# Optimization experiments

Hardware: AMD Instinct MI355X
Metric: run time of the kernel (lower is better)

Reference implementation:

```python
import jax, jax.numpy as jnp
import numpy as np

N = 20000    # num nodes
E = 320000   # num edges (also rows of edge_type, SPN line-graph style)
F = 64       # num_features
HID = 64     # hidden_channels
HEADS = 4    # gatv2_heads
NC = 2       # num_classes
PH = 128     # proxy hidden size
SLOPE = 0.2  # PyG GATv2 leaky_relu negative slope


def gatv2(feat, src, dst, wl, wr, att, b, num_nodes, concat):
    # GATv2Conv (PyG semantics, add_self_loops=True, dropout off in eval)
    H, C = att.shape
    xl = (feat @ wl).reshape(-1, H, C)
    xr = (feat @ wr).reshape(-1, H, C)
    loops = jnp.arange(num_nodes, dtype=src.dtype)
    s = jnp.concatenate([src, loops])
    d = jnp.concatenate([dst, loops])
    e = jax.nn.leaky_relu(xl[s] + xr[d], SLOPE)            # [E', H, C]
    logits = jnp.einsum('ehc,hc->eh', e, att)              # [E', H]
    m = jax.ops.segment_max(logits, d, num_segments=num_nodes)
    p = jnp.exp(logits - m[d])
    z = jax.ops.segment_sum(p, d, num_segments=num_nodes)
    alpha = p / z[d]                                       # segment softmax
    out = jax.ops.segment_sum(xl[s] * alpha[:, :, None], d, num_segments=num_nodes)
    out = out.reshape(num_nodes, H * C) if concat else out.mean(axis=1)
    return out + b


def setup_inputs():
    key = jax.random.key(0)
    ks = iter(jax.random.split(key, 32))
    def rn(shape, scale=0.1):
        return jax.random.normal(next(ks), shape, dtype=jnp.float32) * scale
    return {
        'x': rn((N, F), 1.0),
        'edge_type': rn((E, F), 1.0),
        'edge_index': jax.random.randint(next(ks), (2, E), 0, N, dtype=jnp.int32),
        'n1_wl': rn((F, HEADS * HID)), 'n1_wr': rn((F, HEADS * HID)),
        'n1_att': rn((HEADS, HID)), 'n1_b': jnp.zeros((HEADS * HID,), jnp.float32),
        'n2_wl': rn((HEADS * HID, HID)), 'n2_wr': rn((HEADS * HID, HID)),
        'n2_att': rn((1, HID)), 'n2_b': jnp.zeros((HID,), jnp.float32),
        'e1_wl': rn((F, HEADS * HID)), 'e1_wr': rn((F, HEADS * HID)),
        'e1_att': rn((HEADS, HID)), 'e1_b': jnp.zeros((HEADS * HID,), jnp.float32),
        'e2_wl': rn((HEADS * HID, HID)), 'e2_wr': rn((HEADS * HID, HID)),
        'e2_att': rn((1, HID)), 'e2_b': jnp.zeros((HID,), jnp.float32),
        'crf_wu': rn((HID, NC)), 'crf_bu': jnp.zeros((NC,), jnp.float32),
        'crf_wp': rn((HID, NC)),
        'px_w1': rn((HID, PH)), 'px_b1': jnp.zeros((PH,), jnp.float32),
        'px_w2': rn((PH, NC)), 'px_b2': jnp.zeros((NC,), jnp.float32),
    }


def reference(x, edge_type, edge_index, n1_wl, n1_wr, n1_att, n1_b, n2_wl, n2_wr, n2_att, n2_b,
              e1_wl, e1_wr, e1_att, e1_b, e2_wl, e2_wr, e2_att, e2_b,
              crf_wu, crf_bu, crf_wp, px_w1, px_b1, px_w2, px_b2):
    src, dst = edge_index[0], edge_index[1]
    # node GNN: GATv2 -> ELU -> GATv2 (dropout = identity in eval)
    h = jax.nn.elu(gatv2(x, src, dst, n1_wl, n1_wr, n1_att, n1_b, N, True))
    node_repr = gatv2(h, src, dst, n2_wl, n2_wr, n2_att, n2_b, N, False)
    # edge GNN over edge features (E rows, same edge_index, per source code)
    g = jax.nn.elu(gatv2(edge_type, src, dst, e1_wl, e1_wr, e1_att, e1_b, E, True))
    edge_repr = gatv2(g, src, dst, e2_wl, e2_wr, e2_att, e2_b, E, False)
    # CRF head: unary potentials + pairwise messages scattered to dst nodes
    unary = node_repr @ crf_wu + crf_bu
    msg = jax.ops.segment_sum(edge_repr @ crf_wp, dst, num_segments=N)
    crf_out = jax.nn.log_softmax(unary + msg, axis=-1)
    # MLP proxy head
    ph = jax.nn.relu(node_repr @ px_w1 + px_b1)
    proxy_out = ph @ px_w2 + px_b2
    return crf_out, proxy_out
```

## Files before the change

kernel.cpp:

```cpp
#include <hip/hip_runtime.h>
#include <cstddef>
#include <cstdint>

#define N_NODES 20000
#define N_EDGES 320000

typedef __attribute__((ext_vector_type(8))) short bf8_t;
typedef __attribute__((ext_vector_type(4))) float f4_t;
typedef __attribute__((ext_vector_type(2))) float f2_t;
typedef unsigned short bfu;
typedef _Float16 half_t;
typedef __attribute__((ext_vector_type(2))) _Float16 h2_t;
typedef __attribute__((ext_vector_type(4))) _Float16 h4_t;
typedef __attribute__((ext_vector_type(8))) _Float16 h8_t;

__device__ __forceinline__ short f2bf(float f) {
  unsigned u = __float_as_uint(f);
  u += 0x7fff + ((u >> 16) & 1);
  return (short)(u >> 16);
}
__device__ __forceinline__ h2_t leaky_h2(h2_t t) {
  h2_t zero = {(_Float16)0.f, (_Float16)0.f};
  h2_t mx = __builtin_elementwise_max(t, zero);
  h2_t mn = __builtin_elementwise_min(t, zero);
  h2_t c  = {(_Float16)0.2f, (_Float16)0.2f};
  return mn * c + mx;
}
__device__ __forceinline__ float dot2h(h2_t a, h2_t b, float c) {
#if __has_builtin(__builtin_amdgcn_fdot2)
  return __builtin_amdgcn_fdot2(a, b, c, false);
#else
  return c + (float)a.x * (float)b.x + (float)a.y * (float)b.y;
#endif
}

__global__ void count_deg_kernel(const int* __restrict__ dst, int* __restrict__ deg, int e_cnt) {
  int e = blockIdx.x * blockDim.x + threadIdx.x;
  if (e < e_cnt) atomicAdd(&deg[dst[e]], 1);
}

__global__ __launch_bounds__(1024) void scan_kernel(
    const int* __restrict__ deg, int* __restrict__ rowptr,
    int* __restrict__ cursor, int n) {
  __shared__ int sdata[1024];
  const int CH = (n + 1023) / 1024;
  int tid = threadIdx.x;
  int base = tid * CH;
  int loc[20];
  int s = 0;
  for (int j = 0; j < CH; ++j) {
    int idx = base + j;
    int v = (idx < n) ? deg[idx] : 0;
    loc[j] = s;
    s += v;
  }
  sdata[tid] = s;
  __syncthreads();
  for (int off = 1; off < 1024; off <<= 1) {
    int t = (tid >= off) ? sdata[tid - off] : 0;
    __syncthreads();
    sdata[tid] += t;
    __syncthreads();
  }
  int excl = sdata[tid] - s;
  for (int j = 0; j < CH; ++j) {
    int idx = base + j;
    if (idx < n) { int val = excl + loc[j]; rowptr[idx] = val; cursor[idx] = val; }
  }
  if (tid == 0) rowptr[n] = sdata[1023];
}

__global__ void fill_csr_kernel(const int* __restrict__ src, const int* __restrict__ dst,
                                int* __restrict__ cursor, int* __restrict__ csr_src,
                                int* __restrict__ csr_eid, int e_cnt) {
  int e = blockIdx.x * blockDim.x + threadIdx.x;
  if (e < e_cnt) {
    int pos = atomicAdd(&cursor[dst[e]], 1);
    csr_src[pos] = src[e];
    csr_eid[pos] = e;
  }
}

__global__ void prep_all_kernel(
    const float* __restrict__ n1l, const float* __restrict__ n1r,
    const float* __restrict__ e1l, const float* __restrict__ e1r,
    const float* __restrict__ n2l, const float* __restrict__ n2r,
    const float* __restrict__ e2l, const float* __restrict__ e2r,
    const float* __restrict__ b2, const float* __restrict__ wp,
    short* __restrict__ t_n1l, short* __restrict__ t_n1r,
    short* __restrict__ t_e1l, short* __restrict__ t_e1r,
    short* __restrict__ t_n2l, short* __restrict__ t_n2r,
    short* __restrict__ t_e2l, short* __restrict__ t_e2r,
    float* __restrict__ wct, float* __restrict__ pc)
{
  int i = blockIdx.x * blockDim.x + threadIdx.x;
  int seg = i >> 14;
  int j = i & 16383;
  if (seg < 4) {
    const float* srcs[4] = {n1l, n1r, e1l, e1r};
    short* dsts[4] = {t_n1l, t_n1r, t_e1l, t_e1r};
    int n = j >> 6, k = j & 63;
    dsts[seg][n * 64 + k] = f2bf(srcs[seg][k * 256 + n]);
  } else if (seg < 8) {
    const float* srcs[4] = {n2l, n2r, e2l, e2r};
    short* dsts[4] = {t_n2l, t_n2r, t_e2l, t_e2r};
    int n = j >> 8, k = j & 255;
    dsts[seg - 4][n * 256 + k] = f2bf(srcs[seg - 4][k * 64 + n]);
  } else if (seg == 8) {
    if (j < 512) {
      int jj = j & 1;
      int k  = j >> 1;
      float s = 0.f;
      for (int c = 0; c < 64; ++c) s = fmaf(e2l[k * 64 + c], wp[c * 2 + jj], s);
      wct[jj * 256 + k] = s;
    } else if (j < 514) {
      int jj = j - 512;
      float s = 0.f;
      for (int c = 0; c < 64; ++c) s = fmaf(b2[c], wp[c * 2 + jj], s);
      pc[jj] = s;
    }
  }
}

template<int K>
__global__ __launch_bounds__(128) void mfma_proj2_kernel(
    const float* __restrict__ A0,
    const short* __restrict__ Wtl0, const short* __restrict__ Wtr0,
    half_t* __restrict__ xl0, half_t* __restrict__ xr0,
    const float* __restrict__ A1,
    const short* __restrict__ Wtl1, const short* __restrict__ Wtr1,
    half_t* __restrict__ xl1, half_t* __restrict__ xr1,
    int M, int nslices)
{
  constexpr int KC = K / 32;
  int tid = threadIdx.x;
  int w = tid >> 6, lane = tid & 63, quad = lane >> 4, l15 = lane & 15;
  int row_base = (int)blockIdx.x * 64 + w * 32;
  int y = (int)blockIdx.y;
  int z = (int)blockIdx.z;
  const float* A = z ? A1 : A0;
  bool is_l = y < nslices;
  const short* Wt = z ? (is_l ? Wtl1 : Wtr1) : (is_l ? Wtl0 : Wtr0);
  half_t* dst = z ? (is_l ? xl1 : xr1) : (is_l ? xl0 : xr0);
  int cb = (is_l ? y : y - nslices) * 64;
  int STR = nslices * 64;

  bf8_t a[2][KC];
  #pragma unroll
  for (int rt = 0; rt < 2; ++rt) {
    int r = row_base + rt * 16 + l15;
    int rc = r < M ? r : M - 1;
    const float* ap = A + (size_t)rc * K + quad * 8;
    #pragma unroll
    for (int kc = 0; kc < KC; ++kc) {
      float4 v0 = *(const float4*)(ap + kc * 32);
      float4 v1 = *(const float4*)(ap + kc * 32 + 4);
      bf8_t f;
      f[0] = f2bf(v0.x); f[1] = f2bf(v0.y); f[2] = f2bf(v0.z); f[3] = f2bf(v0.w);
      f[4] = f2bf(v1.x); f[5] = f2bf(v1.y); f[6] = f2bf(v1.z); f[7] = f2bf(v1.w);
      a[rt][kc] = f;
    }
  }

  #pragma unroll
  for (int nt = 0; nt < 4; ++nt) {
    f4_t acc0 = {0.f, 0.f, 0.f, 0.f};
    f4_t acc1 = {0.f, 0.f, 0.f, 0.f};
    const short* wb = Wt + (size_t)(cb + nt * 16 + l15) * K + quad * 8;
    #pragma unroll
    for (int kc = 0; kc < KC; ++kc) {
      bf8_t wf = *(const bf8_t*)(wb + kc * 32);
      acc0 = __builtin_amdgcn_mfma_f32_16x16x32_bf16(wf, a[0][kc], acc0, 0, 0, 0);
      acc1 = __builtin_amdgcn_mfma_f32_16x16x32_bf16(wf, a[1][kc], acc1, 0, 0, 0);
    }
    #pragma unroll
    for (int rt = 0; rt < 2; ++rt) {
      f4_t acc = rt == 0 ? acc0 : acc1;
      int row = row_base + rt * 16 + l15;
      if (row >= M) continue;
      int col = cb + nt * 16 + quad * 4;
      h4_t pk;
      pk[0] = (_Float16)acc[0]; pk[1] = (_Float16)acc[1];
      pk[2] = (_Float16)acc[2]; pk[3] = (_Float16)acc[3];
      *(h4_t*)&dst[(size_t)row * STR + col] = pk;
    }
  }
}

template<int KIN>
__device__ __forceinline__ void gemm_body(
    const float* __restrict__ A, const float* __restrict__ W, int wld, int cb,
    int block_m, int M, float (&acc)[8][4],
    float (*As)[128 + 4], float (*Ws)[64 + 4])
{
  int tid = threadIdx.x;
  int tx = tid & 15;
  int ty = tid >> 4;
  #pragma unroll
  for (int i = 0; i < 8; ++i)
    #pragma unroll
    for (int j = 0; j < 4; ++j) acc[i][j] = 0.f;

  for (int k0 = 0; k0 < KIN; k0 += 16) {
    #pragma unroll
    for (int rep = 0; rep < 2; ++rep) {
      int ar = (tid >> 2) + rep * 64;
      int ak = (tid & 3) * 4;
      int gr = block_m + ar;
      float4 v = make_float4(0.f, 0.f, 0.f, 0.f);
      if (gr < M) v = *(const float4*)&A[(size_t)gr * KIN + k0 + ak];
      As[ak + 0][ar] = v.x; As[ak + 1][ar] = v.y;
      As[ak + 2][ar] = v.z; As[ak + 3][ar] = v.w;
    }
    {
      int wr = tid >> 4;
      int wc = (tid & 15) * 4;
      float4 v = *(const float4*)&W[(size_t)(k0 + wr) * wld + cb + wc];
      Ws[wr][wc + 0] = v.x; Ws[wr][wc + 1] = v.y;
      Ws[wr][wc + 2] = v.z; Ws[wr][wc + 3] = v.w;
    }
    __syncthreads();
    #pragma unroll
    for (int k = 0; k < 16; ++k) {
      float a[8], w[4];
      #pragma unroll
      for (int i = 0; i < 8; ++i) a[i] = As[k][ty * 8 + i];
      #pragma unroll
      for (int j = 0; j < 4; ++j) w[j] = Ws[k][tx * 4 + j];
      #pragma unroll
      for (int i = 0; i < 8; ++i)
        #pragma unroll
        for (int j = 0; j < 4; ++j) acc[i][j] = fmaf(a[i], w[j], acc[i][j]);
    }
    __syncthreads();
  }
}

template<int KIN, int MODE>
__global__ __launch_bounds__(256) void gemm64_kernel(
    const float* __restrict__ A, const float* __restrict__ W, int wld,
    const float* __restrict__ bias, float* __restrict__ out, int old, int M)
{
  __shared__ float As[16][128 + 4];
  __shared__ float Ws[16][64 + 4];
  float acc[8][4];
  int block_m = (int)blockIdx.x * 128;
  int cb = (int)blockIdx.y * 64;
  gemm_body<KIN>(A, W, wld, cb, block_m, M, acc, As, Ws);

  int tid = threadIdx.x;
  int tx = tid & 15, ty = tid >> 4;
  int gc = cb + tx * 4;
  #pragma unroll
  for (int i = 0; i < 8; ++i) {
    int gr = block_m + ty * 8 + i;
    if (gr >= M) continue;
    size_t idx = (size_t)gr * old + gc;
    float t0 = acc[i][0], t1 = acc[i][1], t2 = acc[i][2], t3 = acc[i][3];
    if (MODE == 3) {
      t0 = fmaxf(t0 + bias[gc + 0], 0.f);
      t1 = fmaxf(t1 + bias[gc + 1], 0.f);
      t2 = fmaxf(t2 + bias[gc + 2], 0.f);
      t3 = fmaxf(t3 + bias[gc + 3], 0.f);
    }
    *(float4*)&out[idx] = make_float4(t0, t1, t2, t3);
  }
}

template<int STR, bool ELU, bool FUSEP>
__global__ __launch_bounds__(256) void gat_agg_v6(
    const half_t* __restrict__ xl0, const half_t* __restrict__ xr0,
    const float* __restrict__ att0, const float* __restrict__ bias0,
    float* __restrict__ out0,
    const half_t* __restrict__ xl1, const half_t* __restrict__ xr1,
    const float* __restrict__ att1, const float* __restrict__ bias1,
    float* __restrict__ out1,
    const int* __restrict__ rowptr, const int* __restrict__ csr_src,
    const float* __restrict__ wp, float* __restrict__ pbuf)
{
  constexpr int HEADS = STR / 64;
  constexpr int GRP = N_NODES / 4;
  int tid = threadIdx.x;
  int w = tid >> 6;
  int lane = tid & 63;
  int egrp = lane >> 3;
  int cch  = lane & 7;

  int bid = (int)blockIdx.x;
  int per_chain = HEADS * GRP;
  int chain = bid >= per_chain ? 1 : 0;
  int r = bid - chain * per_chain;
  int head = r / GRP;
  int d = (r - head * GRP) * 4 + w;

  const half_t* xl = chain ? xl1 : xl0;
  const half_t* xr = chain ? xr1 : xr0;
  const float* att = chain ? att1 : att0;
  const float* bias = chain ? bias1 : bias0;

  int row0 = rowptr[d];
  int deg = rowptr[d + 1] - row0;
  int cbase = head * 64 + cch * 8;

  h2_t xr2[4], att2[4];
  {
    h8_t xv = *(const h8_t*)&xr[(unsigned)(d * STR + cbase)];
    xr2[0] = h2_t{xv[0], xv[1]}; xr2[1] = h2_t{xv[2], xv[3]};
    xr2[2] = h2_t{xv[4], xv[5]}; xr2[3] = h2_t{xv[6], xv[7]};
    const float* atp = att + cbase;
    float4 b0 = *(const float4*)(atp);
    float4 b1 = *(const float4*)(atp + 4);
    att2[0] = h2_t{(_Float16)b0.x, (_Float16)b0.y};
    att2[1] = h2_t{(_Float16)b0.z, (_Float16)b0.w};
    att2[2] = h2_t{(_Float16)b1.x, (_Float16)b1.y};
    att2[3] = h2_t{(_Float16)b1.z, (_Float16)b1.w};
  }

  auto ld_idx = [&](int k) -> int {
    int idx = k * 8 + egrp;
    int cl = idx < deg ? idx : (deg > 0 ? deg - 1 : 0);
    int pos = deg > 0 ? row0 + cl : 0;
    int sv = csr_src[pos];
    return idx < deg ? sv : d;
  };

  float zloc;
  f2_t acc4[4];
  {
    h8_t xu = *(const h8_t*)&xl[(unsigned)(d * STR + cbase)];
    h2_t xs[4];
    xs[0] = h2_t{xu[0], xu[1]}; xs[1] = h2_t{xu[2], xu[3]};
    xs[2] = h2_t{xu[4], xu[5]}; xs[3] = h2_t{xu[6], xu[7]};
    float part = 0.f;
    #pragma unroll
    for (int j = 0; j < 4; ++j) part = dot2h(leaky_h2(xs[j] + xr2[j]), att2[j], part);
    part += __shfl_xor(part, 1, 64);
    part += __shfl_xor(part, 2, 64);
    part += __shfl_xor(part, 4, 64);
    float wgt = __expf(part);
    float ws = (egrp == 0) ? wgt : 0.f;
    zloc = ws;
    #pragma unroll
    for (int j = 0; j < 4; ++j) {
      f2_t t;
      t.x = (float)xs[j].x * ws;
      t.y = (float)xs[j].y * ws;
      acc4[j] = t;
    }
  }

  int C = (deg + 7) >> 3;
  int s_cur = ld_idx(0);
  h8_t xu_cur = *(const h8_t*)&xl[(unsigned)(s_cur * STR + cbase)];
  int s_nxt = ld_idx(1);
  for (int k = 0; k < C; ++k) {
    h8_t xu_nxt = *(const h8_t*)&xl[(unsigned)(s_nxt * STR + cbase)];
    int s_n2 = ld_idx(k + 2);
    bool valid = (k * 8 + egrp) < deg;
    h2_t xf[4];
    xf[0] = h2_t{xu_cur[0], xu_cur[1]}; xf[1] = h2_t{xu_cur[2], xu_cur[3]};
    xf[2] = h2_t{xu_cur[4], xu_cur[5]}; xf[3] = h2_t{xu_cur[6], xu_cur[7]};
    float part = 0.f;
    #pragma unroll
    for (int i = 0; i < 4; ++i) part = dot2h(leaky_h2(xf[i] + xr2[i]), att2[i], part);
    part += __shfl_xor(part, 1, 64);
    part += __shfl_xor(part, 2, 64);
    part += __shfl_xor(part, 4, 64);
    float wgt = valid ? __expf(part) : 0.f;
    zloc += wgt;
    #pragma unroll
    for (int i = 0; i < 4; ++i) {
      acc4[i].x = fmaf((float)xf[i].x, wgt, acc4[i].x);
      acc4[i].y = fmaf((float)xf[i].y, wgt, acc4[i].y);
    }
    xu_cur = xu_nxt;
    s_nxt = s_n2;
  }

  float a8[8];
  #pragma unroll
  for (int i = 0; i < 4; ++i) { a8[2 * i] = acc4[i].x; a8[2 * i + 1] = acc4[i].y; }
  #pragma unroll
  for (int off = 8; off < 64; off <<= 1) {
    zloc += __shfl_xor(zloc, off, 64);
    #pragma unroll
    for (int i = 0; i < 8; ++i) a8[i] += __shfl_xor(a8[i], off, 64);
  }

  float invz = 1.f / zloc;
  float o[8];
  #pragma unroll
  for (int i = 0; i < 8; ++i) {
    float val = a8[i] * invz + bias[cbase + i];
    if (ELU) val = val > 0.f ? val : __expf(val) - 1.f;
    o[i] = val;
  }

  if (FUSEP && chain) {
    float p0 = 0.f, p1 = 0.f;
    #pragma unroll
    for (int i = 0; i < 8; ++i) {
      float2 wv = *(const float2*)&wp[(cbase + i) * 2];
      p0 = fmaf(o[i], wv.x, p0);
      p1 = fmaf(o[i], wv.y, p1);
    }
    p0 += __shfl_xor(p0, 1, 64); p1 += __shfl_xor(p1, 1, 64);
    p0 += __shfl_xor(p0, 2, 64); p1 += __shfl_xor(p1, 2, 64);
    p0 += __shfl_xor(p0, 4, 64); p1 += __shfl_xor(p1, 4, 64);
    if (lane == 0) *(float2*)&pbuf[2 * d] = make_float2(p0, p1);
  } else if (egrp == 0) {
    float* out = chain ? out1 : out0;
    float* op = out + (size_t)d * STR + cbase;
    *(float4*)(op)     = make_float4(o[0], o[1], o[2], o[3]);
    *(float4*)(op + 4) = make_float4(o[4], o[5], o[6], o[7]);
  }
}

__global__ __launch_bounds__(64) void chunk_fold_kernel(
    const float* __restrict__ A,
    const short* __restrict__ W1t,
    const float* __restrict__ b1,
    const float* __restrict__ WcT,
    const float* __restrict__ pc,
    float* __restrict__ pbufN,
    int Mtot)
{
  int lane = threadIdx.x;
  int quad = lane >> 4;
  int l15 = lane & 15;
  int row_base = (int)blockIdx.x * 64;

  bf8_t a1[4][2];
  #pragma unroll
  for (int rt = 0; rt < 4; ++rt) {
    int r = row_base + rt * 16 + l15;
    int rc = r < Mtot ? r : Mtot - 1;
    const float* ap = A + (size_t)rc * 64 + quad * 8;
    #pragma unroll
    for (int ks = 0; ks < 2; ++ks) {
      float4 v0 = *(const float4*)(ap + ks * 32);
      float4 v1 = *(const float4*)(ap + ks * 32 + 4);
      bf8_t f;
      f[0] = f2bf(v0.x); f[1] = f2bf(v0.y); f[2] = f2bf(v0.z); f[3] = f2bf(v0.w);
      f[4] = f2bf(v1.x); f[5] = f2bf(v1.y); f[6] = f2bf(v1.z); f[7] = f2bf(v1.w);
      a1[rt][ks] = f;
    }
  }

  float p0[4] = {0.f, 0.f, 0.f, 0.f};
  float p1[4] = {0.f, 0.f, 0.f, 0.f};

  #pragma unroll
  for (int cc = 0; cc < 4; ++cc) {
    #pragma unroll
    for (int nt = 0; nt < 4; ++nt) {
      const short* wb = W1t + (cc * 64 + nt * 16 + l15) * 64 + quad * 8;
      bf8_t w0 = *(const bf8_t*)(wb);
      bf8_t w1 = *(const bf8_t*)(wb + 32);
      f4_t g[4];
      #pragma unroll
      for (int rt = 0; rt < 4; ++rt) {
        f4_t z = {0.f, 0.f, 0.f, 0.f};
        z = __builtin_amdgcn_mfma_f32_16x16x32_bf16(w0, a1[rt][0], z, 0, 0, 0);
        z = __builtin_amdgcn_mfma_f32_16x16x32_bf16(w1, a1[rt][1], z, 0, 0, 0);
        g[rt] = z;
      }
      int cbase = cc * 64 + nt * 16 + quad * 4;
      f4_t b4  = *(const f4_t*)&b1[cbase];
      f4_t wc0 = *(const f4_t*)&WcT[cbase];
      f4_t wc1 = *(const f4_t*)&WcT[256 + cbase];
      #pragma unroll
      for (int rt = 0; rt < 4; ++rt) {
        #pragma unroll
        for (int r = 0; r < 4; ++r) {
          float v = g[rt][r] + b4[r];
          v = v > 0.f ? v : __expf(v) - 1.f;
          p0[rt] = fmaf(v, wc0[r], p0[rt]);
          p1[rt] = fmaf(v, wc1[r], p1[rt]);
        }
      }
    }
  }

  #pragma unroll
  for (int off = 16; off < 64; off <<= 1) {
    #pragma unroll
    for (int rt = 0; rt < 4; ++rt) {
      p0[rt] += __shfl_xor(p0[rt], off, 64);
      p1[rt] += __shfl_xor(p1[rt], off, 64);
    }
  }
  if (quad == 0) {
    float c0 = pc[0], c1 = pc[1];
    #pragma unroll
    for (int rt = 0; rt < 4; ++rt) {
      int row = row_base + rt * 16 + l15;
      if (row < Mtot)
        *(float2*)&pbufN[2 * row] = make_float2(p0[rt] + c0, p1[rt] + c1);
    }
  }
}

__global__ void head_kernel(const float* __restrict__ node_repr, const float* __restrict__ ph,
                            const int* __restrict__ rowptr, const int* __restrict__ csr_eid,
                            const float* __restrict__ pbuf, const float* __restrict__ wu,
                            const float* __restrict__ bu, const float* __restrict__ w2,
                            const float* __restrict__ b2, float* __restrict__ out, int n) {
  __shared__ float swu[128];
  __shared__ float sw2[256];
  int tid = threadIdx.x;
  if (tid < 128) swu[tid] = wu[tid];
  sw2[tid] = w2[tid];
  __syncthreads();
  int i = blockIdx.x * blockDim.x + tid;
  if (i >= n) return;
  float m0 = 0.f, m1 = 0.f;
  int r0 = rowptr[i], r1 = rowptr[i + 1];
  int jj = r0;
  for (; jj + 4 <= r1; jj += 4) {
    int e0 = csr_eid[jj + 0], e1 = csr_eid[jj + 1];
    int e2 = csr_eid[jj + 2], e3 = csr_eid[jj + 3];
    float2 q0 = *(const float2*)&pbuf[2 * e0];
    float2 q1 = *(const float2*)&pbuf[2 * e1];
    float2 q2 = *(const float2*)&pbuf[2 * e2];
    float2 q3 = *(const float2*)&pbuf[2 * e3];
    m0 += (q0.x + q1.x) + (q2.x + q3.x);
    m1 += (q0.y + q1.y) + (q2.y + q3.y);
  }
  for (; jj < r1; ++jj) {
    int e = csr_eid[jj];
    float2 q = *(const float2*)&pbuf[2 * e];
    m0 += q.x; m1 += q.y;
  }
  const float* nr = node_repr + (size_t)i * 64;
  float u0 = bu[0], u1 = bu[1];
  #pragma unroll
  for (int k = 0; k < 64; ++k) {
    float v = nr[k];
    u0 = fmaf(v, swu[2 * k + 0], u0);
    u1 = fmaf(v, swu[2 * k + 1], u1);
  }
  float v0 = u0 + m0;
  float v1 = u1 + m1;
  float mx = fmaxf(v0, v1);
  float lse = mx + logf(__expf(v0 - mx) + __expf(v1 - mx));
  out[2 * i + 0] = v0 - lse;
  out[2 * i + 1] = v1 - lse;
  const float* p = ph + (size_t)i * 128;
  float p0 = b2[0], p1 = b2[1];
  #pragma unroll
  for (int k = 0; k < 128; ++k) {
    float v = p[k];
    p0 = fmaf(v, sw2[2 * k + 0], p0);
    p1 = fmaf(v, sw2[2 * k + 1], p1);
  }
  out[2 * n + 2 * i + 0] = p0;
  out[2 * n + 2 * i + 1] = p1;
}

extern "C" void kernel_launch(void* const* d_in, const int* in_sizes, int n_in,
                              void* d_out, int out_size, void* d_ws, size_t ws_size,
                              hipStream_t stream) {
  const int N = N_NODES, E = N_EDGES;
  const float* x         = (const float*)d_in[0];
  const float* edge_type = (const float*)d_in[1];
  const int*   ei        = (const int*)d_in[2];
  const float* n1_wl  = (const float*)d_in[3];
  const float* n1_wr  = (const float*)d_in[4];
  const float* n1_att = (const float*)d_in[5];
  const float* n1_b   = (const float*)d_in[6];
  const float* n2_wl  = (const float*)d_in[7];
  const float* n2_wr  = (const float*)d_in[8];
  const float* n2_att = (const float*)d_in[9];
  const float* n2_b   = (const float*)d_in[10];
  const float* e1_wl  = (const float*)d_in[11];
  const float* e1_wr  = (const float*)d_in[12];
  const float* e1_att = (const float*)d_in[13];
  const float* e1_b   = (const float*)d_in[14];
  const float* e2_wl  = (const float*)d_in[15];
  const float* e2_wr  = (const float*)d_in[16];
  const float* e2_att = (const float*)d_in[17];
  const float* e2_b   = (const float*)d_in[18];
  const float* crf_wu = (const float*)d_in[19];
  const float* crf_bu = (const float*)d_in[20];
  const float* crf_wp = (const float*)d_in[21];
  const float* px_w1  = (const float*)d_in[22];
  const float* px_b1  = (const float*)d_in[23];
  const float* px_w2  = (const float*)d_in[24];
  const float* px_b2  = (const float*)d_in[25];
  float* out = (float*)d_out;
  const int* src = ei;
  const int* dst = ei + E;
  (void)in_sizes; (void)n_in; (void)out_size; (void)ws_size;

  char* ws = (char*)d_ws;
  size_t off = 0;
  auto alloc = [&](size_t bytes) -> void* {
    void* p = ws + off;
    off += (bytes + 255) & ~(size_t)255;
    return p;
  };
  half_t* xl_n  = (half_t*)alloc((size_t)N * 256 * 2);
  half_t* xr_n  = (half_t*)alloc((size_t)N * 256 * 2);
  half_t* xl_e  = (half_t*)alloc((size_t)N * 256 * 2);
  half_t* xr_e  = (half_t*)alloc((size_t)N * 256 * 2);
  float* h_n   = (float*)alloc((size_t)N * 256 * 4);
  float* g_e   = (float*)alloc((size_t)N * 256 * 4);
  half_t* xl2_n = (half_t*)alloc((size_t)N * 64 * 2);
  half_t* xr2_n = (half_t*)alloc((size_t)N * 64 * 2);
  half_t* xl2_e = (half_t*)alloc((size_t)N * 64 * 2);
  half_t* xr2_e = (half_t*)alloc((size_t)N * 64 * 2);
  float* B3    = (float*)alloc((size_t)N * 64 * 4);
  float* pbuf  = (float*)alloc((size_t)E * 2 * 4);
  float* ph    = (float*)(void*)xl_n;
  int* deg     = (int*)alloc((size_t)N * 4);
  int* rowptr  = (int*)alloc((size_t)(N + 1) * 4);
  int* cursor  = (int*)alloc((size_t)N * 4);
  int* csr_src = (int*)alloc((size_t)E * 4);
  int* csr_eid = (int*)alloc((size_t)E * 4);
  short* t_n1l = (short*)alloc((size_t)16384 * 2);
  short* t_n1r = (short*)alloc((size_t)16384 * 2);
  short* t_e1l = (short*)alloc((size_t)16384 * 2);
  short* t_e1r = (short*)alloc((size_t)16384 * 2);
  short* t_n2l = (short*)alloc((size_t)16384 * 2);
  short* t_n2r = (short*)alloc((size_t)16384 * 2);
  short* t_e2l = (short*)alloc((size_t)16384 * 2);
  short* t_e2r = (short*)alloc((size_t)16384 * 2);
  float* WcT   = (float*)alloc((size_t)2 * 256 * 4);
  float* pcv   = (float*)alloc((size_t)2 * 4);

  const int EB = (E + 255) / 256;
  const int NB = (N + 127) / 128;
  const int PB = (N + 63) / 64;
  const int Mhigh = E - N;
  const int CFB = (Mhigh + 63) / 64;
  const int GRP = N / 4;

  hipMemsetAsync(deg, 0, (size_t)N * 4, stream);
  count_deg_kernel<<<EB, 256, 0, stream>>>(dst, deg, E);
  scan_kernel<<<1, 1024, 0, stream>>>(deg, rowptr, cursor, N);
  fill_csr_kernel<<<EB, 256, 0, stream>>>(src, dst, cursor, csr_src, csr_eid, E);
  prep_all_kernel<<<515, 256, 0, stream>>>(n1_wl, n1_wr, e1_wl, e1_wr,
                                           n2_wl, n2_wr, e2_wl, e2_wr,
                                           e2_b, crf_wp,
                                           t_n1l, t_n1r, t_e1l, t_e1r,
                                           t_n2l, t_n2r, t_e2l, t_e2r, WcT, pcv);

  mfma_proj2_kernel<64><<<dim3(PB, 8, 2), 128, 0, stream>>>(
      x, t_n1l, t_n1r, xl_n, xr_n,
      edge_type, t_e1l, t_e1r, xl_e, xr_e, N, 4);
  gat_agg_v6<256, true, false><<<2 * 4 * GRP, 256, 0, stream>>>(
      xl_n, xr_n, n1_att, n1_b, h_n,
      xl_e, xr_e, e1_att, e1_b, g_e, rowptr, csr_src, nullptr, nullptr);

  mfma_proj2_kernel<256><<<dim3(PB, 2, 2), 128, 0, stream>>>(
      h_n, t_n2l, t_n2r, xl2_n, xr2_n,
      g_e, t_e2l, t_e2r, xl2_e, xr2_e, N, 1);
  gat_agg_v6<64, false, true><<<2 * GRP, 256, 0, stream>>>(
      xl2_n, xr2_n, n2_att, n2_b, B3,
      xl2_e, xr2_e, e2_att, e2_b, nullptr, rowptr, csr_src, crf_wp, pbuf);

  chunk_fold_kernel<<<CFB, 64, 0, stream>>>(edge_type + (size_t)N * 64, t_e1l,
                                            e1_b, WcT, pcv, pbuf + 2 * (size_t)N, Mhigh);

  gemm64_kernel<64, 3><<<dim3(NB, 2), 256, 0, stream>>>(B3, px_w1, 128, px_b1, ph, 128, N);
  head_kernel<<<(N + 255) / 256, 256, 0, stream>>>(B3, ph, rowptr, csr_eid, pbuf,
                                                   crf_wu, crf_bu, px_w2, px_b2, out, N);
}
```

Before: 452.7 us.

## Split leaky-relu into linear plus abs terms, precompute linear logits in projection

Rewrites leaky_relu(t) as 0.6*t + 0.4*|t|, so the linear part of the attention logit becomes att·xl[s] + att·xr[d], computed per node in the MFMA projection epilogue and stored in small buffers. The aggregation kernels then only compute the abs term with a bitmask. Layer 1 is restructured so one wave handles all four heads for a destination with two edge groups instead of one block per head, which cuts repeated index loads. It adds extra per-row scalar loads and writes, and reuses pbuf and xr_n storage as scratch for the new logit buffers. The scan kernel also gets a compile-time chunk count and unrolling.

```diff
diff --git a/kernel.cpp b/kernel.cpp
--- a/kernel.cpp
+++ b/kernel.cpp
@@ -19,12 +19,9 @@
   u += 0x7fff + ((u >> 16) & 1);
   return (short)(u >> 16);
 }
-__device__ __forceinline__ h2_t leaky_h2(h2_t t) {
-  h2_t zero = {(_Float16)0.f, (_Float16)0.f};
-  h2_t mx = __builtin_elementwise_max(t, zero);
-  h2_t mn = __builtin_elementwise_min(t, zero);
-  h2_t c  = {(_Float16)0.2f, (_Float16)0.2f};
-  return mn * c + mx;
+__device__ __forceinline__ h2_t abs_h2(h2_t t) {
+  unsigned u = __builtin_bit_cast(unsigned, t) & 0x7fff7fffu;
+  return __builtin_bit_cast(h2_t, u);
 }
 __device__ __forceinline__ float dot2h(h2_t a, h2_t b, float c) {
 #if __has_builtin(__builtin_amdgcn_fdot2)
@@ -43,11 +40,12 @@
     const int* __restrict__ deg, int* __restrict__ rowptr,
     int* __restrict__ cursor, int n) {
   __shared__ int sdata[1024];
-  const int CH = (n + 1023) / 1024;
+  constexpr int CH = (N_NODES + 1023) / 1024;
   int tid = threadIdx.x;
   int base = tid * CH;
-  int loc[20];
+  int loc[CH];
   int s = 0;
+  #pragma unroll
   for (int j = 0; j < CH; ++j) {
     int idx = base + j;
     int v = (idx < n) ? deg[idx] : 0;
@@ -63,6 +61,7 @@
     __syncthreads();
   }
   int excl = sdata[tid] - s;
+  #pragma unroll
   for (int j = 0; j < CH; ++j) {
     int idx = base + j;
     if (idx < n) { int val = excl + loc[j]; rowptr[idx] = val; cursor[idx] = val; }
@@ -130,6 +129,9 @@
     const float* __restrict__ A1,
     const short* __restrict__ Wtl1, const short* __restrict__ Wtr1,
     half_t* __restrict__ xl1, half_t* __restrict__ xr1,
+    const float* __restrict__ att0, const float* __restrict__ att1,
+    float* __restrict__ ll0, float* __restrict__ lr0,
+    float* __restrict__ ll1, float* __restrict__ lr1,
     int M, int nslices)
 {
   constexpr int KC = K / 32;
@@ -142,7 +144,11 @@
   bool is_l = y < nslices;
   const short* Wt = z ? (is_l ? Wtl1 : Wtr1) : (is_l ? Wtl0 : Wtr0);
   half_t* dst = z ? (is_l ? xl1 : xr1) : (is_l ? xl0 : xr0);
-  int cb = (is_l ? y : y - nslices) * 64;
+  const float* att = z ? att1 : att0;
+  float* lin = z ? (is_l ? ll1 : lr1) : (is_l ? ll0 : lr0);
+  int head = is_l ? y : y - nslices;
+  int cb = head * 64;
+  const float* atp = att + head * 64;
   int STR = nslices * 64;
 
   bf8_t a[2][KC];
@@ -162,6 +168,7 @@
     }
   }
 
+  float lacc0 = 0.f, lacc1 = 0.f;
   #pragma unroll
   for (int nt = 0; nt < 4; ++nt) {
     f4_t acc0 = {0.f, 0.f, 0.f, 0.f};
@@ -173,6 +180,9 @@
       acc0 = __builtin_amdgcn_mfma_f32_16x16x32_bf16(wf, a[0][kc], acc0, 0, 0, 0);
       acc1 = __builtin_amdgcn_mfma_f32_16x16x32_bf16(wf, a[1][kc], acc1, 0, 0, 0);
     }
+    f4_t av = *(const f4_t*)(atp + nt * 16 + quad * 4);
+    lacc0 += acc0[0] * av[0] + acc0[1] * av[1] + acc0[2] * av[2] + acc0[3] * av[3];
+    lacc1 += acc1[0] * av[0] + acc1[1] * av[1] + acc1[2] * av[2] + acc1[3] * av[3];
     #pragma unroll
     for (int rt = 0; rt < 2; ++rt) {
       f4_t acc = rt == 0 ? acc0 : acc1;
@@ -184,6 +194,14 @@
       pk[2] = (_Float16)acc[2]; pk[3] = (_Float16)acc[3];
       *(h4_t*)&dst[(size_t)row * STR + col] = pk;
     }
+  }
+  lacc0 += __shfl_xor(lacc0, 16, 64); lacc0 += __shfl_xor(lacc0, 32, 64);
+  lacc1 += __shfl_xor(lacc1, 16, 64); lacc1 += __shfl_xor(lacc1, 32, 64);
+  if (quad == 0) {
+    int r0 = row_base + l15;
+    int r1 = row_base + 16 + l15;
+    if (r0 < M) lin[(size_t)r0 * nslices + head] = 0.6f * lacc0;
+    if (r1 < M) lin[(size_t)r1 * nslices + head] = 0.6f * lacc1;
   }
 }
 
@@ -267,54 +285,176 @@
   }
 }
 
-template<int STR, bool ELU, bool FUSEP>
-__global__ __launch_bounds__(256) void gat_agg_v6(
+__global__ __launch_bounds__(256) void gat_agg_l1(
     const half_t* __restrict__ xl0, const half_t* __restrict__ xr0,
     const float* __restrict__ att0, const float* __restrict__ bias0,
     float* __restrict__ out0,
     const half_t* __restrict__ xl1, const half_t* __restrict__ xr1,
     const float* __restrict__ att1, const float* __restrict__ bias1,
     float* __restrict__ out1,
+    const float* __restrict__ ll0, const float* __restrict__ lr0,
+    const float* __restrict__ ll1, const float* __restrict__ lr1,
+    const int* __restrict__ rowptr, const int* __restrict__ csr_src)
+{
+  constexpr int GRP = N_NODES / 4;
+  int tid = threadIdx.x;
+  int w = tid >> 6, lane = tid & 63;
+  int egrp = lane >> 5;
+  int head = (lane >> 3) & 3;
+  int coff = (lane & 31) * 8;
+  int bid = (int)blockIdx.x;
+  int chain = bid >= GRP ? 1 : 0;
+  int d = (bid - chain * GRP) * 4 + w;
+
+  const half_t* xl = chain ? xl1 : xl0;
+  const half_t* xr = chain ? xr1 : xr0;
+  const float* att = chain ? att1 : att0;
+  const float* bias = chain ? bias1 : bias0;
+  const float* linl = chain ? ll1 : ll0;
+  const float* linr = chain ? lr1 : lr0;
+  float* out = chain ? out1 : out0;
+
+  int row0 = rowptr[d];
+  int deg = rowptr[d + 1] - row0;
+
+  h2_t xr2[4], attA[4];
+  {
+    h8_t xv = *(const h8_t*)&xr[(unsigned)(d * 256 + coff)];
+    xr2[0] = h2_t{xv[0], xv[1]}; xr2[1] = h2_t{xv[2], xv[3]};
+    xr2[2] = h2_t{xv[4], xv[5]}; xr2[3] = h2_t{xv[6], xv[7]};
+    const float* atp = att + coff;
+    float4 b0 = *(const float4*)(atp);
+    float4 b1 = *(const float4*)(atp + 4);
+    attA[0] = h2_t{(_Float16)(0.4f * b0.x), (_Float16)(0.4f * b0.y)};
+    attA[1] = h2_t{(_Float16)(0.4f * b0.z), (_Float16)(0.4f * b0.w)};
+    attA[2] = h2_t{(_Float16)(0.4f * b1.x), (_Float16)(0.4f * b1.y)};
+    attA[3] = h2_t{(_Float16)(0.4f * b1.z), (_Float16)(0.4f * b1.w)};
+  }
+  float linr_d = linr[(unsigned)(d * 4 + head)];
+
+  auto ld_idx = [&](int k) -> int {
+    int idx = k * 2 + egrp;
+    int cl = idx < deg ? idx : (deg > 0 ? deg - 1 : 0);
+    int pos = deg > 0 ? row0 + cl : 0;
+    int sv = csr_src[pos];
+    return idx < deg ? sv : d;
+  };
+
+  float zloc, a8[8];
+  {
+    h8_t xu = *(const h8_t*)&xl[(unsigned)(d * 256 + coff)];
+    float part = 0.f;
+    #pragma unroll
+    for (int j = 0; j < 4; ++j) {
+      h2_t t = h2_t{xu[2 * j], xu[2 * j + 1]} + xr2[j];
+      part = dot2h(abs_h2(t), attA[j], part);
+    }
+    part += __shfl_xor(part, 1, 64);
+    part += __shfl_xor(part, 2, 64);
+    part += __shfl_xor(part, 4, 64);
+    part += linl[(unsigned)(d * 4 + head)] + linr_d;
+    float wgt = __expf(part);
+    float ws = (egrp == 0) ? wgt : 0.f;
+    zloc = ws;
+    #pragma unroll
+    for (int i = 0; i < 8; ++i) a8[i] = (float)xu[i] * ws;
+  }
+
+  int C = (deg + 1) >> 1;
+  int s_cur = ld_idx(0);
+  h8_t xu_cur = *(const h8_t*)&xl[(unsigned)(s_cur * 256 + coff)];
+  float lin_cur = linl[(unsigned)(s_cur * 4 + head)];
+  int s_nxt = ld_idx(1);
+  for (int k = 0; k < C; ++k) {
+    h8_t xu_nxt = *(const h8_t*)&xl[(unsigned)(s_nxt * 256 + coff)];
+    float lin_nxt = linl[(unsigned)(s_nxt * 4 + head)];
+    int s_n2 = ld_idx(k + 2);
+    bool valid = (k * 2 + egrp) < deg;
+    float part = 0.f;
+    #pragma unroll
+    for (int j = 0; j < 4; ++j) {
+      h2_t t = h2_t{xu_cur[2 * j], xu_cur[2 * j + 1]} + xr2[j];
+      part = dot2h(abs_h2(t), attA[j], part);
+    }
+    part += __shfl_xor(part, 1, 64);
+    part += __shfl_xor(part, 2, 64);
+    part += __shfl_xor(part, 4, 64);
+    part += lin_cur + linr_d;
+    float wgt = valid ? __expf(part) : 0.f;
+    zloc += wgt;
+    #pragma unroll
+    for (int i = 0; i < 8; ++i) a8[i] = fmaf((float)xu_cur[i], wgt, a8[i]);
+    xu_cur = xu_nxt; lin_cur = lin_nxt; s_nxt = s_n2;
+  }
+
+  zloc += __shfl_xor(zloc, 32, 64);
+  #pragma unroll
+  for (int i = 0; i < 8; ++i) a8[i] += __shfl_xor(a8[i], 32, 64);
+
+  if (egrp == 0) {
+    float invz = 1.f / zloc;
+    const float* bp = bias + coff;
+    float4 c0 = *(const float4*)(bp);
+    float4 c1 = *(const float4*)(bp + 4);
+    float o[8];
+    o[0] = a8[0] * invz + c0.x; o[1] = a8[1] * invz + c0.y;
+    o[2] = a8[2] * invz + c0.z; o[3] = a8[3] * invz + c0.w;
+    o[4] = a8[4] * invz + c1.x; o[5] = a8[5] * invz + c1.y;
+    o[6] = a8[6] * invz + c1.z; o[7] = a8[7] * invz + c1.w;
+    #pragma unroll
+    for (int i = 0; i < 8; ++i) o[i] = o[i] > 0.f ? o[i] : __expf(o[i]) - 1.f;
+    float* op = out + (size_t)d * 256 + coff;
+    *(float4*)(op)     = make_float4(o[0], o[1], o[2], o[3]);
+    *(float4*)(op + 4) = make_float4(o[4], o[5], o[6], o[7]);
+  }
+}
+
+__global__ __launch_bounds__(256) void gat_agg_l2(
+    const half_t* __restrict__ xl0, const half_t* __restrict__ xr0,
+    const float* __restrict__ att0, const float* __restrict__ bias0,
+    float* __restrict__ out0,
+    const half_t* __restrict__ xl1, const half_t* __restrict__ xr1,
+    const float* __restrict__ att1, const float* __restrict__ bias1,
+    const float* __restrict__ ll0, const float* __restrict__ lr0,
+    const float* __restrict__ ll1, const float* __restrict__ lr1,
     const int* __restrict__ rowptr, const int* __restrict__ csr_src,
     const float* __restrict__ wp, float* __restrict__ pbuf)
 {
-  constexpr int HEADS = STR / 64;
   constexpr int GRP = N_NODES / 4;
   int tid = threadIdx.x;
   int w = tid >> 6;
   int lane = tid & 63;
   int egrp = lane >> 3;
   int cch  = lane & 7;
-
   int bid = (int)blockIdx.x;
-  int per_chain = HEADS * GRP;
-  int chain = bid >= per_chain ? 1 : 0;
-  int r = bid - chain * per_chain;
-  int head = r / GRP;
-  int d = (r - head * GRP) * 4 + w;
+  int chain = bid >= GRP ? 1 : 0;
+  int d = (bid - chain * GRP) * 4 + w;
 
   const half_t* xl = chain ? xl1 : xl0;
   const half_t* xr = chain ? xr1 : xr0;
   const float* att = chain ? att1 : att0;
   const float* bias = chain ? bias1 : bias0;
+  const float* linl = chain ? ll1 : ll0;
+  const float* linr = chain ? lr1 : lr0;
 
   int row0 = rowptr[d];
   int deg = rowptr[d + 1] - row0;
-  int cbase = head * 64 + cch * 8;
-
-  h2_t xr2[4], att2[4];
+  int cbase = cch * 8;
+
+  h2_t xr2[4], attA[4];
   {
-    h8_t xv = *(const h8_t*)&xr[(unsigned)(d * STR + cbase)];
+    h8_t xv = *(const h8_t*)&xr[(unsigned)(d * 64 + cbase)];
     xr2[0] = h2_t{xv[0], xv[1]}; xr2[1] = h2_t{xv[2], xv[3]};
     xr2[2] = h2_t{xv[4], xv[5]}; xr2[3] = h2_t{xv[6], xv[7]};
     const float* atp = att + cbase;
     float4 b0 = *(const float4*)(atp);
     float4 b1 = *(const float4*)(atp + 4);
-    att2[0] = h2_t{(_Float16)b0.x, (_Float16)b0.y};
-    att2[1] = h2_t{(_Float16)b0.z, (_Float16)b0.w};
-    att2[2] = h2_t{(_Float16)b1.x, (_Float16)b1.y};
-    att2[3] = h2_t{(_Float16)b1.z, (_Float16)b1.w};
-  }
+    attA[0] = h2_t{(_Float16)(0.4f * b0.x), (_Float16)(0.4f * b0.y)};
+    attA[1] = h2_t{(_Float16)(0.4f * b0.z), (_Float16)(0.4f * b0.w)};
+    attA[2] = h2_t{(_Float16)(0.4f * b1.x), (_Float16)(0.4f * b1.y)};
+    attA[3] = h2_t{(_Float16)(0.4f * b1.z), (_Float16)(0.4f * b1.w)};
+  }
+  float linr_d = linr[d];
 
   auto ld_idx = [&](int k) -> int {
     int idx = k * 8 + egrp;
@@ -324,62 +464,53 @@
     return idx < deg ? sv : d;
   };
 
-  float zloc;
-  f2_t acc4[4];
+  float zloc, a8[8];
   {
-    h8_t xu = *(const h8_t*)&xl[(unsigned)(d * STR + cbase)];
-    h2_t xs[4];
-    xs[0] = h2_t{xu[0], xu[1]}; xs[1] = h2_t{xu[2], xu[3]};
-    xs[2] = h2_t{xu[4], xu[5]}; xs[3] = h2_t{xu[6], xu[7]};
+    h8_t xu = *(const h8_t*)&xl[(unsigned)(d * 64 + cbase)];
     float part = 0.f;
     #pragma unroll
-    for (int j = 0; j < 4; ++j) part = dot2h(leaky_h2(xs[j] + xr2[j]), att2[j], part);
+    for (int j = 0; j < 4; ++j) {
+      h2_t t = h2_t{xu[2 * j], xu[2 * j + 1]} + xr2[j];
+      part = dot2h(abs_h2(t), attA[j], part);
+    }
     part += __shfl_xor(part, 1, 64);
     part += __shfl_xor(part, 2, 64);
     part += __shfl_xor(part, 4, 64);
+    part += linl[d] + linr_d;
     float wgt = __expf(part);
     float ws = (egrp == 0) ? wgt : 0.f;
     zloc = ws;
     #pragma unroll
-    for (int j = 0; j < 4; ++j) {
-      f2_t t;
-      t.x = (float)xs[j].x * ws;
-      t.y = (float)xs[j].y * ws;
-      acc4[j] = t;
-    }
+    for (int i = 0; i < 8; ++i) a8[i] = (float)xu[i] * ws;
   }
 
   int C = (deg + 7) >> 3;
   int s_cur = ld_idx(0);
-  h8_t xu_cur = *(const h8_t*)&xl[(unsigned)(s_cur * STR + cbase)];
+  h8_t xu_cur = *(const h8_t*)&xl[(unsigned)(s_cur * 64 + cbase)];
+  float lin_cur = linl[s_cur];
   int s_nxt = ld_idx(1);
   for (int k = 0; k < C; ++k) {
-    h8_t xu_nxt = *(const h8_t*)&xl[(unsigned)(s_nxt * STR + cbase)];
+    h8_t xu_nxt = *(const h8_t*)&xl[(unsigned)(s_nxt * 64 + cbase)];
+    float lin_nxt = linl[s_nxt];
     int s_n2 = ld_idx(k + 2);
     bool valid = (k * 8 + egrp) < deg;
-    h2_t xf[4];
-    xf[0] = h2_t{xu_cur[0], xu_cur[1]}; xf[1] = h2_t{xu_cur[2], xu_cur[3]};
-    xf[2] = h2_t{xu_cur[4], xu_cur[5]}; xf[3] = h2_t{xu_cur[6], xu_cur[7]};
     float part = 0.f;
     #pragma unroll
-    for (int i = 0; i < 4; ++i) part = dot2h(leaky_h2(xf[i] + xr2[i]), att2[i], part);
+    for (int j = 0; j < 4; ++j) {
+      h2_t t = h2_t{xu_cur[2 * j], xu_cur[2 * j + 1]} + xr2[j];
+      part = dot2h(abs_h2(t), attA[j], part);
+    }
     part += __shfl_xor(part, 1, 64);
     part += __shfl_xor(part, 2, 64);
     part += __shfl_xor(part, 4, 64);
+    part += lin_cur + linr_d;
     float wgt = valid ? __expf(part) : 0.f;
     zloc += wgt;
     #pragma unroll
-    for (int i = 0; i < 4; ++i) {
-      acc4[i].x = fmaf((float)xf[i].x, wgt, acc4[i].x);
-      acc4[i].y = fmaf((float)xf[i].y, wgt, acc4[i].y);
-    }
-    xu_cur = xu_nxt;
-    s_nxt = s_n2;
-  }
-
-  float a8[8];
-  #pragma unroll
-  for (int i = 0; i < 4; ++i) { a8[2 * i] = acc4[i].x; a8[2 * i + 1] = acc4[i].y; }
+    for (int i = 0; i < 8; ++i) a8[i] = fmaf((float)xu_cur[i], wgt, a8[i]);
+    xu_cur = xu_nxt; lin_cur = lin_nxt; s_nxt = s_n2;
+  }
+
   #pragma unroll
   for (int off = 8; off < 64; off <<= 1) {
     zloc += __shfl_xor(zloc, off, 64);
@@ -390,13 +521,9 @@
   float invz = 1.f / zloc;
   float o[8];
   #pragma unroll
-  for (int i = 0; i < 8; ++i) {
-    float val = a8[i] * invz + bias[cbase + i];
-    if (ELU) val = val > 0.f ? val : __expf(val) - 1.f;
-    o[i] = val;
-  }
-
-  if (FUSEP && chain) {
+  for (int i = 0; i < 8; ++i) o[i] = a8[i] * invz + bias[cbase + i];
+
+  if (chain) {
     float p0 = 0.f, p1 = 0.f;
     #pragma unroll
     for (int i = 0; i < 8; ++i) {
@@ -409,8 +536,7 @@
     p0 += __shfl_xor(p0, 4, 64); p1 += __shfl_xor(p1, 4, 64);
     if (lane == 0) *(float2*)&pbuf[2 * d] = make_float2(p0, p1);
   } else if (egrp == 0) {
-    float* out = chain ? out1 : out0;
-    float* op = out + (size_t)d * STR + cbase;
+    float* op = out0 + (size_t)d * 64 + cbase;
     *(float4*)(op)     = make_float4(o[0], o[1], o[2], o[3]);
     *(float4*)(op + 4) = make_float4(o[4], o[5], o[6], o[7]);
   }
@@ -628,6 +754,15 @@
   short* t_e2r = (short*)alloc((size_t)16384 * 2);
   float* WcT   = (float*)alloc((size_t)2 * 256 * 4);
   float* pcv   = (float*)alloc((size_t)2 * 4);
+  float* l1ln = pbuf;
+  float* l1rn = pbuf + 80000;
+  float* l1le = pbuf + 160000;
+  float* l1re = pbuf + 240000;
+  float* l2base = (float*)(void*)xr_n;
+  float* l2ln = l2base;
+  float* l2rn = l2base + 20000;
+  float* l2le = l2base + 40000;
+  float* l2re = l2base + 60000;
 
   const int EB = (E + 255) / 256;
   const int NB = (N + 127) / 128;
@@ -648,17 +783,21 @@
 
   mfma_proj2_kernel<64><<<dim3(PB, 8, 2), 128, 0, stream>>>(
       x, t_n1l, t_n1r, xl_n, xr_n,
-      edge_type, t_e1l, t_e1r, xl_e, xr_e, N, 4);
-  gat_agg_v6<256, true, false><<<2 * 4 * GRP, 256, 0, stream>>>(
+      edge_type, t_e1l, t_e1r, xl_e, xr_e,
+      n1_att, e1_att, l1ln, l1rn, l1le, l1re, N, 4);
+  gat_agg_l1<<<2 * GRP, 256, 0, stream>>>(
       xl_n, xr_n, n1_att, n1_b, h_n,
-      xl_e, xr_e, e1_att, e1_b, g_e, rowptr, csr_src, nullptr, nullptr);
+      xl_e, xr_e, e1_att, e1_b, g_e,
+      l1ln, l1rn, l1le, l1re, rowptr, csr_src);
 
   mfma_proj2_kernel<256><<<dim3(PB, 2, 2), 128, 0, stream>>>(
       h_n, t_n2l, t_n2r, xl2_n, xr2_n,
-      g_e, t_e2l, t_e2r, xl2_e, xr2_e, N, 1);
-  gat_agg_v6<64, false, true><<<2 * GRP, 256, 0, stream>>>(
+      g_e, t_e2l, t_e2r, xl2_e, xr2_e,
+      n2_att, e2_att, l2ln, l2rn, l2le, l2re, N, 1);
+  gat_agg_l2<<<2 * GRP, 256, 0, stream>>>(
       xl2_n, xr2_n, n2_att, n2_b, B3,
-      xl2_e, xr2_e, e2_att, e2_b, nullptr, rowptr, csr_src, crf_wp, pbuf);
+      xl2_e, xr2_e, e2_att, e2_b,
+      l2ln, l2rn, l2le, l2re, rowptr, csr_src, crf_wp, pbuf);
 
   chunk_fold_kernel<<<CFB, 64, 0, stream>>>(edge_type + (size_t)N * 64, t_e1l,
                                             e1_b, WcT, pcv, pbuf + 2 * (size_t)N, Mhigh);
```

Result: faster. 422.7 us (-6.6%).
